# Kernel optimization log

Hardware: AMD Instinct MI355X
Metric: run time of the kernel (lower is better)

The kernel has to match this reference:

```python
import jax, jax.numpy as jnp
import numpy as np

N, E, B = 50000, 600000, 512
IN, HID, META = 128, 128, 27


def _gcn_layer(h_in, W, b, src, dst, norm, n_nodes):
    # GCNConv: out = scatter_add_{dst}( norm * (x W)[src] ) + b
    h = h_in @ W  # [N, HID]
    msg = h[src] * norm[:, None]  # [E+N, HID] gather + scale
    out = jax.ops.segment_sum(msg, dst, num_segments=n_nodes)
    return out + b


def setup_inputs() -> dict:
    key = jax.random.key(0)
    ks = jax.random.split(key, 16)
    x = jax.random.normal(ks[0], (N, IN), dtype=jnp.float32)
    edge_index = jax.random.randint(ks[1], (2, E), 0, N, dtype=jnp.int64)
    batch = jnp.sort(jax.random.randint(ks[2], (N,), 0, B, dtype=jnp.int64))
    metadata = jax.random.normal(ks[3], (B, META), dtype=jnp.float32)
    def glorot(k, shape):
        lim = np.sqrt(6.0 / (shape[0] + shape[1]))
        return jax.random.uniform(k, shape, jnp.float32, -lim, lim)
    params = {
        'W1': glorot(ks[4], (IN, HID)),  'b1': jnp.zeros((HID,), jnp.float32),
        'W2': glorot(ks[5], (HID, HID)), 'b2': jnp.zeros((HID,), jnp.float32),
        'W3': glorot(ks[6], (HID, HID)), 'b3': jnp.zeros((HID,), jnp.float32),
        'Wh1': glorot(ks[7], (HID + META, HID)), 'bh1': jnp.zeros((HID,), jnp.float32),
        'Wh2': glorot(ks[8], (HID, 1)),  'bh2': jnp.zeros((1,), jnp.float32),
    }
    return {'x': x, 'edge_index': edge_index, 'batch': batch, 'metadata': metadata, **params}


def reference(x, edge_index, batch, metadata, W1, b1, W2, b2, W3, b3, Wh1, bh1, Wh2, bh2):
    n_nodes = x.shape[0]
    # add self loops (PyG GCNConv default)
    loops = jnp.arange(n_nodes, dtype=edge_index.dtype)
    src = jnp.concatenate([edge_index[0], loops])
    dst = jnp.concatenate([edge_index[1], loops])
    # symmetric degree normalization D^{-1/2} A_hat D^{-1/2}
    deg = jax.ops.segment_sum(jnp.ones_like(dst, dtype=x.dtype), dst, num_segments=n_nodes)
    dinv = jax.lax.rsqrt(jnp.maximum(deg, 1.0))  # self-loops guarantee deg >= 1
    norm = dinv[src] * dinv[dst]  # [E+N]
    h = jax.nn.relu(_gcn_layer(x, W1, b1, src, dst, norm, n_nodes))
    h = jax.nn.relu(_gcn_layer(h, W2, b2, src, dst, norm, n_nodes))
    h = jax.nn.relu(_gcn_layer(h, W3, b3, src, dst, norm, n_nodes))
    # global mean pool over graphs
    n_graphs = metadata.shape[0]
    summed = jax.ops.segment_sum(h, batch, num_segments=n_graphs)  # [B, HID]
    counts = jax.ops.segment_sum(jnp.ones((n_nodes,), x.dtype), batch, num_segments=n_graphs)
    emb = summed / jnp.maximum(counts, 1.0)[:, None]
    # MLP head
    z = jnp.concatenate([emb, metadata], axis=1)  # [B, HID+META]
    z = jax.nn.relu(z @ Wh1 + bh1)
    return z @ Wh2 + bh2  # [B, 1] raw logits
```

## Files before the change

### kernel.cpp

```cpp
#include <hip/hip_runtime.h>

#define NN 50000
#define NE 600000
#define NB 512
#define HD 128
#define NMETA 27
#define CAP 64

typedef __attribute__((ext_vector_type(8))) short short8;
typedef __attribute__((ext_vector_type(4))) float f32x4;

__device__ __forceinline__ float relu(float x) { return fmaxf(x, 0.0f); }

__device__ __forceinline__ unsigned short f2bf(float f) {
    unsigned u = __float_as_uint(f);
    unsigned r = u + 0x7FFFu + ((u >> 16) & 1u);
    return (unsigned short)(r >> 16);
}
__device__ __forceinline__ float bf2f(unsigned short v) {
    return __uint_as_float(((unsigned)v) << 16);
}
__device__ __forceinline__ float dinv_of(int c) { return rsqrtf((float)c + 1.0f); }

__global__ __launch_bounds__(256) void k_build(const int* __restrict__ src, const int* __restrict__ dst,
                                               int* __restrict__ cnt, int* __restrict__ csr) {
    int e = blockIdx.x * 256 + threadIdx.x;
    if (e >= NE) return;
    int s = src[e], d = dst[e];
    int pos = atomicAdd(&cnt[d], 1);
    if (pos < CAP) csr[(size_t)d * CAP + pos] = s;
}

__global__ __launch_bounds__(256) void k_castWt3(const float* __restrict__ W1, const float* __restrict__ W2,
                                                 const float* __restrict__ W3, unsigned short* __restrict__ Wt1,
                                                 unsigned short* __restrict__ Wt2, unsigned short* __restrict__ Wt3) {
    int i = blockIdx.x * 256 + threadIdx.x;
    if (i >= 3 * HD * HD) return;
    int which = i / (HD * HD);
    int r = i - which * (HD * HD);
    int k = r >> 7, n = r & 127;
    const float* W = (which == 0) ? W1 : (which == 1) ? W2 : W3;
    unsigned short* Wt = (which == 0) ? Wt1 : (which == 1) ? Wt2 : Wt3;
    Wt[n * HD + k] = f2bf(W[r]);
}

__global__ __launch_bounds__(256) void k_gemm_x(const float* __restrict__ X,
                                                const unsigned short* __restrict__ Wt,
                                                const int* __restrict__ cnt,
                                                unsigned short* __restrict__ T) {
    __shared__ unsigned short Ws[HD * HD];
    char* wsb = (char*)Ws;
    for (int i = threadIdx.x; i < HD * HD / 8; i += 256) {
        short8 v = ((const short8*)Wt)[i];
        int byte = i * 16;
        *(short8*)(wsb + (byte ^ (((byte >> 8) & 7) << 4))) = v;
    }
    __syncthreads();

    const int wave = threadIdx.x >> 6;
    const int lane = threadIdx.x & 63;
    const int lr = lane & 15;
    const int kh = lane >> 4;
    const int r0 = blockIdx.x * 64 + wave * 16;
    const float* arow = X + (size_t)min(r0 + lr, NN - 1) * HD + kh * 8;

    f32x4 acc[8] = {};
#pragma unroll
    for (int kk = 0; kk < 4; ++kk) {
        float4 a0 = *reinterpret_cast<const float4*>(arow + kk * 32);
        float4 a1 = *reinterpret_cast<const float4*>(arow + kk * 32 + 4);
        short8 af;
        af[0] = (short)f2bf(a0.x); af[1] = (short)f2bf(a0.y);
        af[2] = (short)f2bf(a0.z); af[3] = (short)f2bf(a0.w);
        af[4] = (short)f2bf(a1.x); af[5] = (short)f2bf(a1.y);
        af[6] = (short)f2bf(a1.z); af[7] = (short)f2bf(a1.w);
#pragma unroll
        for (int n = 0; n < 8; ++n) {
            int byte = (n * 16 + lr) * 256 + kk * 64 + kh * 16;
            short8 bf = *(const short8*)(wsb + (byte ^ (((byte >> 8) & 7) << 4)));
            acc[n] = __builtin_amdgcn_mfma_f32_16x16x32_bf16(af, bf, acc[n], 0, 0, 0);
        }
    }
    float dv[4];
#pragma unroll
    for (int r = 0; r < 4; ++r) {
        int row = r0 + kh * 4 + r;
        dv[r] = (row < NN) ? dinv_of(cnt[row]) : 0.0f;
    }
#pragma unroll
    for (int n = 0; n < 8; ++n) {
#pragma unroll
        for (int r = 0; r < 4; ++r) {
            int row = r0 + kh * 4 + r;
            if (row < NN) T[(size_t)row * HD + n * 16 + lr] = f2bf(acc[n][r] * dv[r]);
        }
    }
}

template <int MODE>
__global__ __launch_bounds__(512, 8) void k_fused(const int* __restrict__ cnt, const int* __restrict__ csr,
                                                  const unsigned short* __restrict__ Tin,
                                                  const float* __restrict__ b, const unsigned short* __restrict__ Wt,
                                                  unsigned short* __restrict__ Out, const int* __restrict__ batch,
                                                  float* __restrict__ embsum) {
    __shared__ char smem[32 * 132 * 4 + 128];
    char* hsb = smem;
    float* hsf = (float*)smem;
    int* sg = (int*)(smem + 32 * 132 * 4);

    const int rl  = threadIdx.x >> 4;
    const int l16 = threadIdx.x & 15;
    const int row = blockIdx.x * 32 + rl;
    const int c   = l16 * 8;

    if (MODE == 2 && threadIdx.x < 32) {
        int rr = blockIdx.x * 32 + threadIdx.x;
        sg[threadIdx.x] = (rr < NN) ? batch[rr] : -1;
    }

    float acc[8] = {};

    if (row < NN) {
        const int deg = min(cnt[row], CAP);
        const int* eb = csr + (size_t)row * CAP;
        int j = 0;
        int sA0, sA1, sA2, sA3, sB0, sB1, sB2, sB3;
        bool haveA = (j + 3 < deg);
        if (haveA) { sA0 = eb[j]; sA1 = eb[j + 1]; sA2 = eb[j + 2]; sA3 = eb[j + 3]; }
        while (haveA) {
            const int jn = j + 4;
            const bool haveB = (jn + 3 < deg);
            if (haveB) { sB0 = eb[jn]; sB1 = eb[jn + 1]; sB2 = eb[jn + 2]; sB3 = eb[jn + 3]; }
            short8 t0 = *reinterpret_cast<const short8*>(Tin + (size_t)sA0 * HD + c);
            short8 t1 = *reinterpret_cast<const short8*>(Tin + (size_t)sA1 * HD + c);
            short8 t2 = *reinterpret_cast<const short8*>(Tin + (size_t)sA2 * HD + c);
            short8 t3 = *reinterpret_cast<const short8*>(Tin + (size_t)sA3 * HD + c);
#pragma unroll
            for (int i = 0; i < 8; ++i) {
                acc[i] += bf2f((unsigned short)t0[i]);
                acc[i] += bf2f((unsigned short)t1[i]);
                acc[i] += bf2f((unsigned short)t2[i]);
                acc[i] += bf2f((unsigned short)t3[i]);
            }
            j = jn;
            sA0 = sB0; sA1 = sB1; sA2 = sB2; sA3 = sB3;
            haveA = haveB;
        }
        for (; j < deg; ++j) {
            int s = eb[j];
            short8 tv = *reinterpret_cast<const short8*>(Tin + (size_t)s * HD + c);
#pragma unroll
            for (int i = 0; i < 8; ++i) acc[i] += bf2f((unsigned short)tv[i]);
        }
        const float di = dinv_of(deg);
        short8 ts = *reinterpret_cast<const short8*>(Tin + (size_t)row * HD + c);
        float4 bb0 = *reinterpret_cast<const float4*>(b + c);
        float4 bb1 = *reinterpret_cast<const float4*>(b + c + 4);
        float h[8];
#pragma unroll
        for (int i = 0; i < 8; ++i) {
            float bbv = (i < 4) ? (&bb0.x)[i] : (&bb1.x)[i - 4];
            h[i] = relu(fmaf(di, acc[i] + bf2f((unsigned short)ts[i]), bbv));
        }
        if (MODE == 1) {
            short8 o;
#pragma unroll
            for (int i = 0; i < 8; ++i) o[i] = (short)f2bf(h[i]);
            int byte0 = rl * 256 + c * 2;
            *(short8*)(hsb + (byte0 ^ (((byte0 >> 8) & 7) << 4))) = o;
        } else {
            *(float4*)(&hsf[rl * 132 + c])     = make_float4(h[0], h[1], h[2], h[3]);
            *(float4*)(&hsf[rl * 132 + c + 4]) = make_float4(h[4], h[5], h[6], h[7]);
        }
    } else {
        if (MODE == 1) {
            short8 z = {0, 0, 0, 0, 0, 0, 0, 0};
            int byte0 = rl * 256 + c * 2;
            *(short8*)(hsb + (byte0 ^ (((byte0 >> 8) & 7) << 4))) = z;
        } else {
            float4 z = make_float4(0.f, 0.f, 0.f, 0.f);
            *(float4*)(&hsf[rl * 132 + c])     = z;
            *(float4*)(&hsf[rl * 132 + c + 4]) = z;
        }
    }
    __syncthreads();

    if (MODE == 1) {
        const int w = threadIdx.x >> 6;
        const int lane = threadIdx.x & 63;
        const int lr = lane & 15;
        const int kh = lane >> 4;
        f32x4 acc0 = {}, acc1 = {};
#pragma unroll
        for (int kk = 0; kk < 4; ++kk) {
            short8 bf = *reinterpret_cast<const short8*>(Wt + (size_t)(w * 16 + lr) * HD + kk * 32 + kh * 8);
            int byteA = lr * 256 + kk * 64 + kh * 16;
            int byteB = (16 + lr) * 256 + kk * 64 + kh * 16;
            short8 af0 = *(const short8*)(hsb + (byteA ^ (((byteA >> 8) & 7) << 4)));
            short8 af1 = *(const short8*)(hsb + (byteB ^ (((byteB >> 8) & 7) << 4)));
            acc0 = __builtin_amdgcn_mfma_f32_16x16x32_bf16(af0, bf, acc0, 0, 0, 0);
            acc1 = __builtin_amdgcn_mfma_f32_16x16x32_bf16(af1, bf, acc1, 0, 0, 0);
        }
#pragma unroll
        for (int r = 0; r < 4; ++r) {
            int row0 = blockIdx.x * 32 + kh * 4 + r;
            int row1 = row0 + 16;
            if (row0 < NN) Out[(size_t)row0 * HD + w * 16 + lr] = f2bf(acc0[r] * dinv_of(cnt[row0]));
            if (row1 < NN) Out[(size_t)row1 * HD + w * 16 + lr] = f2bf(acc1[r] * dinv_of(cnt[row1]));
        }
    } else {
        if (threadIdx.x < HD) {
            const int cc = threadIdx.x;
            float a = 0.f;
            int gcur = -1;
#pragma unroll 8
            for (int r = 0; r < 32; ++r) {
                int g = sg[r];
                if (g != gcur) {
                    if (gcur >= 0) atomicAdd(&embsum[gcur * HD + cc], a);
                    a = 0.f;
                    gcur = g;
                }
                a += hsf[r * 132 + cc];
            }
            if (gcur >= 0) atomicAdd(&embsum[gcur * HD + cc], a);
        }
    }
}

__global__ __launch_bounds__(128) void k_head(const float* __restrict__ embsum, const int* __restrict__ batch,
                                              const float* __restrict__ meta,
                                              const float* __restrict__ Wh1, const float* __restrict__ bh1,
                                              const float* __restrict__ Wh2, const float* __restrict__ bh2,
                                              float* __restrict__ out) {
    int g = blockIdx.x;
    int c = threadIdx.x;
    int l = 0, r = NN;
    while (l < r) { int m = (l + r) >> 1; if (batch[m] < g) l = m + 1; else r = m; }
    int lo = l;
    r = NN;
    while (l < r) { int m = (l + r) >> 1; if (batch[m] < g + 1) l = m + 1; else r = m; }
    int hi = l;
    float rcp = 1.0f / (float)max(hi - lo, 1);

    __shared__ float emb[HD];
    __shared__ float mt[NMETA];
    emb[c] = embsum[g * HD + c] * rcp;
    if (c < NMETA) mt[c] = meta[g * NMETA + c];
    __syncthreads();

    float z = bh1[c];
    float z0 = 0.f, z1 = 0.f, z2 = 0.f, z3 = 0.f;
    for (int k = 0; k < HD; k += 4) {
        z0 = fmaf(emb[k],     Wh1[k * HD + c],       z0);
        z1 = fmaf(emb[k + 1], Wh1[(k + 1) * HD + c], z1);
        z2 = fmaf(emb[k + 2], Wh1[(k + 2) * HD + c], z2);
        z3 = fmaf(emb[k + 3], Wh1[(k + 3) * HD + c], z3);
    }
    for (int k = 0; k < NMETA; ++k) z = fmaf(mt[k], Wh1[(HD + k) * HD + c], z);
    z += (z0 + z1) + (z2 + z3);
    z = relu(z);
    __shared__ float red[HD];
    red[c] = z * Wh2[c];
    __syncthreads();
    for (int st = 64; st > 0; st >>= 1) {
        if (c < st) red[c] += red[c + st];
        __syncthreads();
    }
    if (c == 0) out[g] = red[0] + bh2[0];
}

extern "C" void kernel_launch(void* const* d_in, const int* in_sizes, int n_in,
                              void* d_out, int out_size, void* d_ws, size_t ws_size,
                              hipStream_t stream) {
    const float* x     = (const float*)d_in[0];
    const int*   ei    = (const int*)d_in[1];
    const int*   src   = ei;
    const int*   dst   = ei + NE;
    const int*   batch = (const int*)d_in[2];
    const float* meta  = (const float*)d_in[3];
    const float* W1 = (const float*)d_in[4];  const float* b1 = (const float*)d_in[5];
    const float* W2 = (const float*)d_in[6];  const float* b2 = (const float*)d_in[7];
    const float* W3 = (const float*)d_in[8];  const float* b3 = (const float*)d_in[9];
    const float* Wh1 = (const float*)d_in[10]; const float* bh1 = (const float*)d_in[11];
    const float* Wh2 = (const float*)d_in[12]; const float* bh2 = (const float*)d_in[13];
    float* out = (float*)d_out;

    int*   cnt    = (int*)d_ws;
    float* embsum = (float*)(cnt + NN);
    int*   csr    = (int*)(embsum + NB * HD);
    unsigned short* Ta  = (unsigned short*)(csr + (size_t)NN * CAP);
    unsigned short* Tc  = Ta + (size_t)NN * HD;
    unsigned short* Hb  = Tc + (size_t)NN * HD;
    unsigned short* Wt1 = Hb + (size_t)NN * HD;
    unsigned short* Wt2 = Wt1 + HD * HD;
    unsigned short* Wt3 = Wt2 + HD * HD;

    const int GEMM_GRID  = (NN + 63) / 64;
    const int FUSED_GRID = (NN + 31) / 32;
    const int CWT_GRID   = (3 * HD * HD + 255) / 256;

    hipMemsetAsync(cnt, 0, NN * sizeof(int) + NB * HD * sizeof(float), stream);
    k_build<<<(NE + 255) / 256, 256, 0, stream>>>(src, dst, cnt, csr);
    k_castWt3<<<CWT_GRID, 256, 0, stream>>>(W1, W2, W3, Wt1, Wt2, Wt3);

    k_gemm_x<<<GEMM_GRID, 256, 0, stream>>>(x, Wt1, cnt, Ta);
    k_fused<1><<<FUSED_GRID, 512, 0, stream>>>(cnt, csr, Ta, b1, Wt2, Tc, nullptr, nullptr);
    k_fused<1><<<FUSED_GRID, 512, 0, stream>>>(cnt, csr, Tc, b2, Wt3, Ta, nullptr, nullptr);
    k_fused<2><<<FUSED_GRID, 512, 0, stream>>>(cnt, csr, Ta, b3, nullptr, nullptr, batch, embsum);

    k_head<<<NB, 128, 0, stream>>>(embsum, batch, meta, Wh1, bh1, Wh2, bh2, out);
}
```

Baseline: 262.7 us.

## Compress CSR to 16-bit indices, merge build and cast, unroll gather by 8

Stores neighbor indices as 16-bit values, which halves CSR traffic, and loads 8 indices per vector load so the gather loop is unrolled 8-wide with tree-summed accumulation. It merges the edge-build and weight-cast kernels into one launch, adds nontemporal loads and stores, and lowers the occupancy hint in launch_bounds from 8 to 6. The 16-bit indices overflow because N=50000 is below 65536 only barely: unsigned short holds up to 65535, so they fit. The 8-wide vector load of indices requires the CSR rows to be 16-byte aligned, which holds because each row is 64 entries of 2 bytes.

```diff
diff --git a/kernel.cpp b/kernel.cpp
--- a/kernel.cpp
+++ b/kernel.cpp
@@ -8,6 +8,7 @@
 #define CAP 64
 
 typedef __attribute__((ext_vector_type(8))) short short8;
+typedef __attribute__((ext_vector_type(8))) unsigned short ushort8v;
 typedef __attribute__((ext_vector_type(4))) float f32x4;
 
 __device__ __forceinline__ float relu(float x) { return fmaxf(x, 0.0f); }
@@ -22,26 +23,29 @@
 }
 __device__ __forceinline__ float dinv_of(int c) { return rsqrtf((float)c + 1.0f); }
 
-__global__ __launch_bounds__(256) void k_build(const int* __restrict__ src, const int* __restrict__ dst,
-                                               int* __restrict__ cnt, int* __restrict__ csr) {
-    int e = blockIdx.x * 256 + threadIdx.x;
-    if (e >= NE) return;
-    int s = src[e], d = dst[e];
-    int pos = atomicAdd(&cnt[d], 1);
-    if (pos < CAP) csr[(size_t)d * CAP + pos] = s;
-}
-
-__global__ __launch_bounds__(256) void k_castWt3(const float* __restrict__ W1, const float* __restrict__ W2,
-                                                 const float* __restrict__ W3, unsigned short* __restrict__ Wt1,
-                                                 unsigned short* __restrict__ Wt2, unsigned short* __restrict__ Wt3) {
-    int i = blockIdx.x * 256 + threadIdx.x;
-    if (i >= 3 * HD * HD) return;
-    int which = i / (HD * HD);
-    int r = i - which * (HD * HD);
-    int k = r >> 7, n = r & 127;
-    const float* W = (which == 0) ? W1 : (which == 1) ? W2 : W3;
-    unsigned short* Wt = (which == 0) ? Wt1 : (which == 1) ? Wt2 : Wt3;
-    Wt[n * HD + k] = f2bf(W[r]);
+__global__ __launch_bounds__(256) void k_buildcast(const int* __restrict__ src, const int* __restrict__ dst,
+                                                   int* __restrict__ cnt, unsigned short* __restrict__ csr,
+                                                   const float* __restrict__ W1, const float* __restrict__ W2,
+                                                   const float* __restrict__ W3, unsigned short* __restrict__ Wt1,
+                                                   unsigned short* __restrict__ Wt2, unsigned short* __restrict__ Wt3) {
+    const int b = blockIdx.x;
+    if (b < 192) {
+        int i = b * 256 + threadIdx.x;
+        int which = i / (HD * HD);
+        int r = i - which * (HD * HD);
+        int k = r >> 7, n = r & 127;
+        const float* W = (which == 0) ? W1 : (which == 1) ? W2 : W3;
+        unsigned short* Wt = (which == 0) ? Wt1 : (which == 1) ? Wt2 : Wt3;
+        Wt[n * HD + k] = f2bf(W[r]);
+    } else {
+        int e = (b - 192) * 256 + threadIdx.x;
+        if (e < NE) {
+            int s = src[e], d = dst[e];
+            int pos = atomicAdd(&cnt[d], 1);
+            if (pos < CAP)
+                __builtin_nontemporal_store((unsigned short)s, &csr[(size_t)d * CAP + pos]);
+        }
+    }
 }
 
 __global__ __launch_bounds__(256) void k_gemm_x(const float* __restrict__ X,
@@ -98,7 +102,7 @@
 }
 
 template <int MODE>
-__global__ __launch_bounds__(512, 8) void k_fused(const int* __restrict__ cnt, const int* __restrict__ csr,
+__global__ __launch_bounds__(512, 6) void k_fused(const int* __restrict__ cnt, const unsigned short* __restrict__ csr,
                                                   const unsigned short* __restrict__ Tin,
                                                   const float* __restrict__ b, const unsigned short* __restrict__ Wt,
                                                   unsigned short* __restrict__ Out, const int* __restrict__ batch,
@@ -122,33 +126,43 @@
 
     if (row < NN) {
         const int deg = min(cnt[row], CAP);
-        const int* eb = csr + (size_t)row * CAP;
+        const unsigned short* eb = csr + (size_t)row * CAP;
         int j = 0;
-        int sA0, sA1, sA2, sA3, sB0, sB1, sB2, sB3;
-        bool haveA = (j + 3 < deg);
-        if (haveA) { sA0 = eb[j]; sA1 = eb[j + 1]; sA2 = eb[j + 2]; sA3 = eb[j + 3]; }
-        while (haveA) {
-            const int jn = j + 4;
-            const bool haveB = (jn + 3 < deg);
-            if (haveB) { sB0 = eb[jn]; sB1 = eb[jn + 1]; sB2 = eb[jn + 2]; sB3 = eb[jn + 3]; }
-            short8 t0 = *reinterpret_cast<const short8*>(Tin + (size_t)sA0 * HD + c);
-            short8 t1 = *reinterpret_cast<const short8*>(Tin + (size_t)sA1 * HD + c);
-            short8 t2 = *reinterpret_cast<const short8*>(Tin + (size_t)sA2 * HD + c);
-            short8 t3 = *reinterpret_cast<const short8*>(Tin + (size_t)sA3 * HD + c);
+        const int nfull = deg & ~7;
+        for (; j < nfull; j += 8) {
+            ushort8v iv = __builtin_nontemporal_load(reinterpret_cast<const ushort8v*>(eb + j));
+            short8 t0 = *reinterpret_cast<const short8*>(Tin + (size_t)iv[0] * HD + c);
+            short8 t1 = *reinterpret_cast<const short8*>(Tin + (size_t)iv[1] * HD + c);
+            short8 t2 = *reinterpret_cast<const short8*>(Tin + (size_t)iv[2] * HD + c);
+            short8 t3 = *reinterpret_cast<const short8*>(Tin + (size_t)iv[3] * HD + c);
+            short8 t4 = *reinterpret_cast<const short8*>(Tin + (size_t)iv[4] * HD + c);
+            short8 t5 = *reinterpret_cast<const short8*>(Tin + (size_t)iv[5] * HD + c);
+            short8 t6 = *reinterpret_cast<const short8*>(Tin + (size_t)iv[6] * HD + c);
+            short8 t7 = *reinterpret_cast<const short8*>(Tin + (size_t)iv[7] * HD + c);
 #pragma unroll
             for (int i = 0; i < 8; ++i) {
-                acc[i] += bf2f((unsigned short)t0[i]);
-                acc[i] += bf2f((unsigned short)t1[i]);
-                acc[i] += bf2f((unsigned short)t2[i]);
-                acc[i] += bf2f((unsigned short)t3[i]);
+                float s01 = bf2f((unsigned short)t0[i]) + bf2f((unsigned short)t1[i]);
+                float s23 = bf2f((unsigned short)t2[i]) + bf2f((unsigned short)t3[i]);
+                float s45 = bf2f((unsigned short)t4[i]) + bf2f((unsigned short)t5[i]);
+                float s67 = bf2f((unsigned short)t6[i]) + bf2f((unsigned short)t7[i]);
+                acc[i] += (s01 + s23) + (s45 + s67);
             }
-            j = jn;
-            sA0 = sB0; sA1 = sB1; sA2 = sB2; sA3 = sB3;
-            haveA = haveB;
+        }
+        if (j + 3 < deg) {
+            short8 t0 = *reinterpret_cast<const short8*>(Tin + (size_t)eb[j + 0] * HD + c);
+            short8 t1 = *reinterpret_cast<const short8*>(Tin + (size_t)eb[j + 1] * HD + c);
+            short8 t2 = *reinterpret_cast<const short8*>(Tin + (size_t)eb[j + 2] * HD + c);
+            short8 t3 = *reinterpret_cast<const short8*>(Tin + (size_t)eb[j + 3] * HD + c);
+#pragma unroll
+            for (int i = 0; i < 8; ++i) {
+                float s01 = bf2f((unsigned short)t0[i]) + bf2f((unsigned short)t1[i]);
+                float s23 = bf2f((unsigned short)t2[i]) + bf2f((unsigned short)t3[i]);
+                acc[i] += s01 + s23;
+            }
+            j += 4;
         }
         for (; j < deg; ++j) {
-            int s = eb[j];
-            short8 tv = *reinterpret_cast<const short8*>(Tin + (size_t)s * HD + c);
+            short8 tv = *reinterpret_cast<const short8*>(Tin + (size_t)eb[j] * HD + c);
 #pragma unroll
             for (int i = 0; i < 8; ++i) acc[i] += bf2f((unsigned short)tv[i]);
         }
@@ -205,8 +219,10 @@
         for (int r = 0; r < 4; ++r) {
             int row0 = blockIdx.x * 32 + kh * 4 + r;
             int row1 = row0 + 16;
-            if (row0 < NN) Out[(size_t)row0 * HD + w * 16 + lr] = f2bf(acc0[r] * dinv_of(cnt[row0]));
-            if (row1 < NN) Out[(size_t)row1 * HD + w * 16 + lr] = f2bf(acc1[r] * dinv_of(cnt[row1]));
+            if (row0 < NN)
+                __builtin_nontemporal_store(f2bf(acc0[r] * dinv_of(cnt[row0])), &Out[(size_t)row0 * HD + w * 16 + lr]);
+            if (row1 < NN)
+                __builtin_nontemporal_store(f2bf(acc1[r] * dinv_of(cnt[row1])), &Out[(size_t)row1 * HD + w * 16 + lr]);
         }
     } else {
         if (threadIdx.x < HD) {
@@ -288,21 +304,19 @@
 
     int*   cnt    = (int*)d_ws;
     float* embsum = (float*)(cnt + NN);
-    int*   csr    = (int*)(embsum + NB * HD);
-    unsigned short* Ta  = (unsigned short*)(csr + (size_t)NN * CAP);
+    unsigned short* csr = (unsigned short*)(embsum + NB * HD);
+    unsigned short* Ta  = csr + (size_t)NN * CAP;
     unsigned short* Tc  = Ta + (size_t)NN * HD;
-    unsigned short* Hb  = Tc + (size_t)NN * HD;
-    unsigned short* Wt1 = Hb + (size_t)NN * HD;
+    unsigned short* Wt1 = Tc + (size_t)NN * HD;
     unsigned short* Wt2 = Wt1 + HD * HD;
     unsigned short* Wt3 = Wt2 + HD * HD;
 
     const int GEMM_GRID  = (NN + 63) / 64;
     const int FUSED_GRID = (NN + 31) / 32;
-    const int CWT_GRID   = (3 * HD * HD + 255) / 256;
+    const int BC_GRID    = 192 + (NE + 255) / 256;
 
     hipMemsetAsync(cnt, 0, NN * sizeof(int) + NB * HD * sizeof(float), stream);
-    k_build<<<(NE + 255) / 256, 256, 0, stream>>>(src, dst, cnt, csr);
-    k_castWt3<<<CWT_GRID, 256, 0, stream>>>(W1, W2, W3, Wt1, Wt2, Wt3);
+    k_buildcast<<<BC_GRID, 256, 0, stream>>>(src, dst, cnt, csr, W1, W2, W3, Wt1, Wt2, Wt3);
 
     k_gemm_x<<<GEMM_GRID, 256, 0, stream>>>(x, Wt1, cnt, Ta);
     k_fused<1><<<FUSED_GRID, 512, 0, stream>>>(cnt, csr, Ta, b1, Wt2, Tc, nullptr, nullptr);
```

Result: slower. 271.8 us (+3.5%).
